# Performance work log

Hardware: AMD Instinct MI355X
Metric: run time of the kernel (lower is better)

Reference implementation:

```python
import jax, jax.numpy as jnp
import numpy as np

H, SK, SV, PK, PV = 12, 16, 16, 4, 8
SCALAR_DIM, PAIR_DIM = 384, 128
SIZES = [SK*H, SK*H, SV*H, PK*H*3, PK*H*3, PV*H*3]  # qkv split sizes
N_LOGITS = 3
SS = (N_LOGITS * SK) ** -0.5                 # scalar logit scale
PS = (N_LOGITS * PK * 4.5) ** -0.5           # point logit scale
PBS = N_LOGITS ** -0.5                       # pair bias scale
EPS = 1e-8


def setup_inputs() -> dict:
    key = jax.random.key(0)
    ks = jax.random.split(key, 16)
    b, n = 1, 768
    scalar_feats = jax.random.normal(ks[0], (b, n, SCALAR_DIM), jnp.float32)
    pair_feats = jax.random.normal(ks[1], (b, n, n, PAIR_DIM), jnp.float32)
    rotations = jax.random.normal(ks[2], (b, n, 3, 3), jnp.float32)
    translations = jax.random.normal(ks[3], (b, n, 3), jnp.float32)
    mask = jnp.ones((b, n), dtype=bool)
    d_qkv = sum(SIZES)
    sc = SCALAR_DIM ** -0.5
    Wqkv = jax.random.normal(ks[4], (SCALAR_DIM, d_qkv), jnp.float32) * sc
    Wpb = jax.random.normal(ks[5], (PAIR_DIM, H), jnp.float32) * PAIR_DIM ** -0.5
    point_weights = jnp.full((1, H, 1, 1), float(np.log(np.e - 1.0)), jnp.float32)
    dim_out = H * (PAIR_DIM + SV + 4 * PV)  # 2112
    Wout = jax.random.normal(ks[6], (dim_out, SCALAR_DIM), jnp.float32) * dim_out ** -0.5
    bout = jnp.zeros((SCALAR_DIM,), jnp.float32)
    Wp1 = jax.random.normal(ks[7], (3 * H, PAIR_DIM), jnp.float32) * (3 * H) ** -0.5
    bp1 = jnp.zeros((PAIR_DIM,), jnp.float32)
    Wp2 = jax.random.normal(ks[8], (PAIR_DIM, PAIR_DIM), jnp.float32) * PAIR_DIM ** -0.5
    bp2 = jnp.zeros((PAIR_DIM,), jnp.float32)
    return dict(scalar_feats=scalar_feats, pair_feats=pair_feats, rotations=rotations,
                translations=translations, mask=mask, Wqkv=Wqkv, Wpb=Wpb,
                point_weights=point_weights, Wout=Wout, bout=bout,
                Wp1=Wp1, bp1=bp1, Wp2=Wp2, bp2=bp2)


def _heads(x, b, n, d):
    # b n (h d) -> b h n d
    return x.reshape(b, n, H, d).transpose(0, 2, 1, 3)


def _merge(x):
    # b h n d -> b n (h d)
    b, h, n, d = x.shape
    return x.transpose(0, 2, 1, 3).reshape(b, n, h * d)


def ipa_forward(scalar_feats, pair_feats, rotations, translations, mask,
                Wqkv, Wpb, point_weights, Wout, bout, Wp1, bp1, Wp2, bp2):
    b, n, _ = scalar_feats.shape
    qkv = scalar_feats @ Wqkv
    offs = np.cumsum([0] + SIZES)
    qs, ks_, vs, qp, kp, vp = [qkv[..., offs[i]:offs[i + 1]] for i in range(6)]
    qs, ks_, vs = _heads(qs, b, n, SK), _heads(ks_, b, n, SK), _heads(vs, b, n, SV)

    def to_global_points(p, d):
        p = p.reshape(b, n, H * d, 3)                       # ... (d c) -> ... d c
        p = jnp.einsum('bixy,bidy->bidx', rotations, p) + translations[:, :, None, :]
        return p.reshape(b, n, H, d, 3).transpose(0, 2, 1, 3, 4)  # b h n d 3

    qp, kp = to_global_points(qp, PK), to_global_points(kp, PK)
    vp = to_global_points(vp, PV)

    scalar_logits = jnp.einsum('bhid,bhjd->bhij', qs, ks_)
    pair_bias = jnp.einsum('bijd,dh->bhij', pair_feats, Wpb)
    point_logits = jnp.einsum('bhidc,bhjdc->bhij', qp, kp) * jax.nn.softplus(point_weights)

    m2 = mask[:, None, :, None] & mask[:, None, None, :]    # b 1 i j
    neg = -jnp.finfo(scalar_logits.dtype).max
    scalar_logits = jnp.where(m2, scalar_logits, neg)
    point_logits = jnp.where(m2, point_logits, neg)
    pair_bias = jnp.where(m2, pair_bias, neg)

    attn = jax.nn.softmax(SS * scalar_logits + PS * point_logits + PBS * pair_bias, axis=-1)

    res_scalar = jnp.einsum('bhij,bhjd->bhid', attn, vs)
    res_pair = jnp.einsum('bhij,bijd->bhid', attn, pair_feats)
    res_pts = jnp.einsum('bhij,bhjdc->bhidc', attn, vp)
    # inverse rigid: R^T (p - t)
    local = jnp.einsum('biyx,bhidy->bhidx', rotations,
                       res_pts - translations[:, None, :, None, :])
    pts_norm = jnp.sqrt(jnp.sum(local ** 2, axis=-1) + EPS)  # safe_norm

    feats = jnp.concatenate([
        _merge(res_scalar),                                   # b n h*SV
        _merge(res_pair),                                     # b n h*PAIR_DIM
        _merge(local.reshape(b, H, n, PV * 3)),               # b n h*PV*3
        _merge(pts_norm),                                     # b n h*PV
    ], axis=-1)
    scalar_out = feats @ Wout + bout

    edge = jnp.concatenate([attn,
                            jax.nn.softmax(point_logits, axis=-1),
                            jax.nn.softmax(scalar_logits, axis=-1)], axis=1)
    edge = edge.transpose(0, 2, 3, 1)                         # b i j (3h)
    pair_out = jax.nn.gelu(edge @ Wp1 + bp1, approximate=False) @ Wp2 + bp2
    return scalar_out, pair_out


def reference(scalar_feats, pair_feats, rotations, translations, mask,
              Wqkv, Wpb, point_weights, Wout, bout, Wp1, bp1, Wp2, bp2):
    return ipa_forward(scalar_feats, pair_feats, rotations, translations, mask,
                       Wqkv, Wpb, point_weights, Wout, bout, Wp1, bp1, Wp2, bp2)
```

## Files before the change

### kernel.cpp

```cpp
#include <hip/hip_runtime.h>
#include <hip/hip_bf16.h>
#include <math.h>

#define NRES 768
#define NH 12
#define DQKV 1152
#define PAIRD 128
#define SCD 384
#define DOUTF 2112

#define SS_C 0.14433756729740643f
#define PS_C 0.13608276348795434f
#define PBS_C 0.5773502691896258f

typedef __attribute__((ext_vector_type(4))) float f32x4;
typedef __attribute__((ext_vector_type(8))) short s16x8;

__device__ __forceinline__ unsigned short f2bf(float x) {
  union { float f; unsigned u; } v; v.f = x;
  unsigned r = (v.u + 0x7fffu + ((v.u >> 16) & 1u)) >> 16;
  return (unsigned short)r;
}
__device__ __forceinline__ float bf2f(unsigned short h) {
  union { unsigned u; float f; } v; v.u = (unsigned)h << 16;
  return v.f;
}

__global__ __launch_bounds__(256) void gemm_bf16(
    const unsigned short* __restrict__ A, const unsigned short* __restrict__ Bt,
    const float* __restrict__ bias, float* __restrict__ C,
    int M, int Nn, int K)
{
  __shared__ __align__(16) unsigned short A_lds[64][72];
  __shared__ __align__(16) unsigned short B_lds[64][72];
  int m0 = blockIdx.y * 64, n0 = blockIdx.x * 64;
  int t = threadIdx.x;
  int lane = t & 63, w = t >> 6;
  int n15 = lane & 15, q = lane >> 4;
  f32x4 acc[4];
#pragma unroll
  for (int nt = 0; nt < 4; ++nt) acc[nt] = (f32x4){0.f, 0.f, 0.f, 0.f};
  for (int k0 = 0; k0 < K; k0 += 64) {
    __syncthreads();
#pragma unroll
    for (int u = 0; u < 2; ++u) {
      int idx = t + u * 256;
      int r = idx >> 3, c = (idx & 7) * 8;
      *(s16x8*)&A_lds[r][c] = *(const s16x8*)&A[(size_t)(m0 + r) * K + k0 + c];
      *(s16x8*)&B_lds[r][c] = *(const s16x8*)&Bt[(size_t)(n0 + r) * K + k0 + c];
    }
    __syncthreads();
#pragma unroll
    for (int ks = 0; ks < 2; ++ks) {
      s16x8 af = *(const s16x8*)&A_lds[w * 16 + n15][ks * 32 + q * 8];
#pragma unroll
      for (int nt = 0; nt < 4; ++nt) {
        s16x8 bf = *(const s16x8*)&B_lds[nt * 16 + n15][ks * 32 + q * 8];
        acc[nt] = __builtin_amdgcn_mfma_f32_16x16x32_bf16(af, bf, acc[nt], 0, 0, 0);
      }
    }
  }
#pragma unroll
  for (int nt = 0; nt < 4; ++nt) {
    int n = n0 + nt * 16 + n15;
    float bv = bias ? bias[n] : 0.f;
#pragma unroll
    for (int r = 0; r < 4; ++r) {
      int m = m0 + w * 16 + q * 4 + r;
      C[(size_t)m * Nn + n] = acc[nt][r] + bv;
    }
  }
}

__global__ __launch_bounds__(256) void prep_wqkv_kernel(
    const float* __restrict__ W, unsigned short* __restrict__ Bt)
{
  __shared__ float tile[32][33];
  int k0 = blockIdx.x * 32, n0 = blockIdx.y * 32;
  int t = threadIdx.x;
  int x = t & 31, y = t >> 5;
#pragma unroll
  for (int r = 0; r < 32; r += 8)
    tile[y + r][x] = W[(size_t)(k0 + y + r) * DQKV + n0 + x];
  __syncthreads();
#pragma unroll
  for (int r = 0; r < 32; r += 8) {
    float v = tile[x][y + r];
    unsigned short hi = f2bf(v);
    unsigned short lo = f2bf(v - bf2f(hi));
    size_t nrow = (size_t)(n0 + y + r) * 1152;
    Bt[nrow + k0 + x]       = hi;
    Bt[nrow + 384 + k0 + x] = lo;
    Bt[nrow + 768 + k0 + x] = hi;
  }
}

__global__ __launch_bounds__(128) void prep_a_kernel(
    const float* __restrict__ A, unsigned short* __restrict__ Ap)
{
  int i = blockIdx.x, t = threadIdx.x;
#pragma unroll
  for (int p = 0; p < 3; ++p) {
    int c = t + p * 128;
    float v = A[(size_t)i * SCD + c];
    unsigned short hi = f2bf(v);
    unsigned short lo = f2bf(v - bf2f(hi));
    size_t row = (size_t)i * 1152;
    Ap[row + c]       = hi;
    Ap[row + 384 + c] = hi;
    Ap[row + 768 + c] = lo;
  }
}

__global__ __launch_bounds__(256) void wt_kernel(
    const float* __restrict__ W, unsigned short* __restrict__ Wt)
{
  __shared__ float tile[32][33];
  int k0 = blockIdx.x * 32, n0 = blockIdx.y * 32;
  int t = threadIdx.x;
  int x = t & 31, y = t >> 5;
#pragma unroll
  for (int r = 0; r < 32; r += 8)
    tile[y + r][x] = W[(size_t)(k0 + y + r) * SCD + n0 + x];
  __syncthreads();
#pragma unroll
  for (int r = 0; r < 32; r += 8)
    Wt[(size_t)(n0 + y + r) * DOUTF + k0 + x] = f2bf(tile[x][y + r]);
}

__global__ __launch_bounds__(192) void points_kernel(
    const float* __restrict__ qkv, const float* __restrict__ rot,
    const float* __restrict__ trans, float* __restrict__ QP,
    float* __restrict__ KP, float* __restrict__ VP, float* __restrict__ Kq)
{
  int i = blockIdx.x;
  int t = threadIdx.x;
  const float* R = rot + (size_t)i * 9;
  const float* T = trans + (size_t)i * 3;
  int base; float* outp;
  if (t < 48) { int h = t >> 2, d = t & 3; base = 576 + (h * 4 + d) * 3;
    outp = QP + ((size_t)h * NRES + i) * 12 + d * 3; }
  else if (t < 96) { int u = t - 48; int h = u >> 2, d = u & 3; base = 720 + (h * 4 + d) * 3;
    outp = KP + ((size_t)h * NRES + i) * 12 + d * 3; }
  else { int u = t - 96; int h = u >> 3, d = u & 7; base = 864 + (h * 8 + d) * 3;
    outp = VP + ((size_t)h * NRES + i) * 24 + d * 3; }
  const float* p = qkv + (size_t)i * DQKV + base;
  float p0 = p[0], p1 = p[1], p2 = p[2];
#pragma unroll
  for (int x = 0; x < 3; ++x)
    outp[x] = R[x * 3 + 0] * p0 + R[x * 3 + 1] * p1 + R[x * 3 + 2] * p2 + T[x];
  {
    int h = t >> 4, d = t & 15;
    Kq[((size_t)h * NRES + i) * 16 + d] = qkv[(size_t)i * DQKV + 192 + h * 16 + d];
  }
}

__global__ __launch_bounds__(256) void vt_kernel(
    const float* __restrict__ qkv, const float* __restrict__ VP,
    unsigned short* __restrict__ Vt)
{
  int b = blockIdx.x;
  int h = b / 48, o = b % 48;
  int t = threadIdx.x;
  for (int p = 0; p < 3; ++p) {
    int j = p * 256 + t;
    float v;
    if (o < 16) v = qkv[(size_t)j * DQKV + 384 + h * 16 + o];
    else if (o < 40) v = VP[((size_t)h * NRES + j) * 24 + (o - 16)];
    else v = 0.f;
    Vt[((size_t)h * 48 + o) * NRES + j] = f2bf(v);
  }
}

__global__ __launch_bounds__(256) void pair_bias_kernel(
    const float* __restrict__ pair, const float* __restrict__ Wpb,
    float* __restrict__ Lb, unsigned short* __restrict__ pair_b)
{
  __shared__ __align__(16) unsigned short Bt[64][136];
  int jt = blockIdx.x, i = blockIdx.y;
  int j0 = jt * 64;
  int t = threadIdx.x;
  int lane = t & 63, w = t >> 6;
  int n15 = lane & 15, q = lane >> 4;
  s16x8 wf[4];
#pragma unroll
  for (int ks = 0; ks < 4; ++ks) {
#pragma unroll
    for (int jj = 0; jj < 8; ++jj) {
      int k = ks * 32 + q * 8 + jj;
      float v = (n15 < 12) ? Wpb[k * 12 + n15] : 0.f;
      wf[ks][jj] = (short)f2bf(v);
    }
  }
  {
    int dq = t & 31, jb = t >> 5;
    for (int p = 0; p < 8; ++p) {
      int j = p * 8 + jb;
      float4 v = *(const float4*)(pair + ((size_t)i * NRES + j0 + j) * PAIRD + dq * 4);
      unsigned lo = (unsigned)f2bf(v.x) | ((unsigned)f2bf(v.y) << 16);
      unsigned hi = (unsigned)f2bf(v.z) | ((unsigned)f2bf(v.w) << 16);
      uint2 pk; pk.x = lo; pk.y = hi;
      *(uint2*)&Bt[j][dq * 4] = pk;
      *(uint2*)&pair_b[((size_t)i * NRES + j0 + j) * PAIRD + dq * 4] = pk;
    }
  }
  __syncthreads();
  f32x4 acc = {0.f, 0.f, 0.f, 0.f};
  int m = w * 16 + n15;
#pragma unroll
  for (int ks = 0; ks < 4; ++ks) {
    s16x8 af = *(const s16x8*)&Bt[m][ks * 32 + q * 8];
    acc = __builtin_amdgcn_mfma_f32_16x16x32_bf16(af, wf[ks], acc, 0, 0, 0);
  }
  if (n15 < 12) {
    int j = j0 + w * 16 + q * 4;
    float4 st; st.x = acc[0]; st.y = acc[1]; st.z = acc[2]; st.w = acc[3];
    *(float4*)(Lb + ((size_t)n15 * NRES + i) * NRES + j) = st;
  }
}

#define RL 4
__global__ __launch_bounds__(256) void logits_softmax_kernel(
    const float* __restrict__ qkv, const float* __restrict__ Kq,
    const float* __restrict__ QP, const float* __restrict__ KP,
    const float* __restrict__ pw, const float* __restrict__ Lb,
    unsigned short* __restrict__ attn_b, unsigned short* __restrict__ sp_b,
    unsigned short* __restrict__ ss_b)
{
  int it = blockIdx.x, h = blockIdx.y;
  int i0 = it * RL;
  int t = threadIdx.x;
  __shared__ float q_sh[RL][28];
  if (t < RL * 28) {
    int r = t / 28, c = t % 28;
    q_sh[r][c] = (c < 16) ? qkv[(size_t)(i0 + r) * DQKV + h * 16 + c]
                          : QP[((size_t)h * NRES + i0 + r) * 12 + (c - 16)];
  }
  __syncthreads();
  float spw = log1pf(expf(pw[h]));
  float s[RL][3], p[RL][3], c[RL][3];
#pragma unroll
  for (int e = 0; e < 3; ++e) {
    int j = t + e * 256;
    float kr[16];
    const float* kq = Kq + ((size_t)h * NRES + j) * 16;
    *(float4*)&kr[0]  = *(const float4*)(kq + 0);
    *(float4*)&kr[4]  = *(const float4*)(kq + 4);
    *(float4*)&kr[8]  = *(const float4*)(kq + 8);
    *(float4*)&kr[12] = *(const float4*)(kq + 12);
    float kp[12];
    const float* kpp = KP + ((size_t)h * NRES + j) * 12;
    *(float4*)&kp[0] = *(const float4*)(kpp + 0);
    *(float4*)&kp[4] = *(const float4*)(kpp + 4);
    *(float4*)&kp[8] = *(const float4*)(kpp + 8);
#pragma unroll
    for (int r = 0; r < RL; ++r) {
      float sv = 0.f;
#pragma unroll
      for (int d = 0; d < 16; ++d) sv += q_sh[r][d] * kr[d];
      float pv = 0.f;
#pragma unroll
      for (int d = 0; d < 12; ++d) pv += q_sh[r][16 + d] * kp[d];
      pv *= spw;
      float bv = Lb[((size_t)h * NRES + i0 + r) * NRES + j];
      s[r][e] = sv; p[r][e] = pv;
      c[r][e] = SS_C * sv + PS_C * pv + PBS_C * bv;
    }
  }
  __shared__ float redm[4][RL][3];
  __shared__ float redsu[4][RL][3];
  int wv = t >> 6;
#pragma unroll
  for (int r = 0; r < RL; ++r) {
    float ms = fmaxf(fmaxf(s[r][0], s[r][1]), s[r][2]);
    float mp = fmaxf(fmaxf(p[r][0], p[r][1]), p[r][2]);
    float mc = fmaxf(fmaxf(c[r][0], c[r][1]), c[r][2]);
#pragma unroll
    for (int o = 32; o > 0; o >>= 1) {
      ms = fmaxf(ms, __shfl_down(ms, o));
      mp = fmaxf(mp, __shfl_down(mp, o));
      mc = fmaxf(mc, __shfl_down(mc, o));
    }
    if ((t & 63) == 0) { redm[wv][r][0] = ms; redm[wv][r][1] = mp; redm[wv][r][2] = mc; }
  }
  __syncthreads();
  float Ms[RL], Mp[RL], Mc[RL];
#pragma unroll
  for (int r = 0; r < RL; ++r) {
    Ms[r] = fmaxf(fmaxf(redm[0][r][0], redm[1][r][0]), fmaxf(redm[2][r][0], redm[3][r][0]));
    Mp[r] = fmaxf(fmaxf(redm[0][r][1], redm[1][r][1]), fmaxf(redm[2][r][1], redm[3][r][1]));
    Mc[r] = fmaxf(fmaxf(redm[0][r][2], redm[1][r][2]), fmaxf(redm[2][r][2], redm[3][r][2]));
  }
#pragma unroll
  for (int r = 0; r < RL; ++r) {
    float sums = 0.f, sump = 0.f, sumc = 0.f;
#pragma unroll
    for (int e = 0; e < 3; ++e) {
      float es = expf(s[r][e] - Ms[r]); s[r][e] = es; sums += es;
      float ep = expf(p[r][e] - Mp[r]); p[r][e] = ep; sump += ep;
      float ec = expf(c[r][e] - Mc[r]); c[r][e] = ec; sumc += ec;
    }
#pragma unroll
    for (int o = 32; o > 0; o >>= 1) {
      sums += __shfl_down(sums, o);
      sump += __shfl_down(sump, o);
      sumc += __shfl_down(sumc, o);
    }
    if ((t & 63) == 0) { redsu[wv][r][0] = sums; redsu[wv][r][1] = sump; redsu[wv][r][2] = sumc; }
  }
  __syncthreads();
#pragma unroll
  for (int r = 0; r < RL; ++r) {
    float rs = 1.f / (redsu[0][r][0] + redsu[1][r][0] + redsu[2][r][0] + redsu[3][r][0]);
    float rp = 1.f / (redsu[0][r][1] + redsu[1][r][1] + redsu[2][r][1] + redsu[3][r][1]);
    float rc = 1.f / (redsu[0][r][2] + redsu[1][r][2] + redsu[2][r][2] + redsu[3][r][2]);
    size_t off = ((size_t)h * NRES + i0 + r) * NRES;
#pragma unroll
    for (int e = 0; e < 3; ++e) {
      int j = t + e * 256;
      ss_b[off + j]   = f2bf(s[r][e] * rs);
      sp_b[off + j]   = f2bf(p[r][e] * rp);
      attn_b[off + j] = f2bf(c[r][e] * rc);
    }
  }
}

__global__ __launch_bounds__(192) void res_sv_kernel(
    const unsigned short* __restrict__ attn, const unsigned short* __restrict__ Vt,
    float* __restrict__ res_sv)
{
  __shared__ __align__(16) unsigned short A_lds[16][72];
  __shared__ __align__(16) unsigned short B_lds[48][72];
  int it = blockIdx.x, h = blockIdx.y;
  int i0 = it * 16;
  int t = threadIdx.x;
  int lane = t & 63, w = t >> 6;
  int n15 = lane & 15, q = lane >> 4;
  f32x4 acc = {0.f, 0.f, 0.f, 0.f};
  for (int jt = 0; jt < 12; ++jt) {
    int j0 = jt * 64;
    __syncthreads();
    for (int idx = t; idx < 512; idx += 192) {
      int r = idx >> 5, j2 = idx & 31;
      *(unsigned*)&A_lds[r][j2 * 2] =
          *(const unsigned*)&attn[((size_t)h * NRES + i0 + r) * NRES + j0 + j2 * 2];
    }
    for (int idx = t; idx < 1536; idx += 192) {
      int o = idx >> 5, j2 = idx & 31;
      *(unsigned*)&B_lds[o][j2 * 2] =
          *(const unsigned*)&Vt[((size_t)h * 48 + o) * NRES + j0 + j2 * 2];
    }
    __syncthreads();
#pragma unroll
    for (int ks = 0; ks < 2; ++ks) {
      s16x8 af = *(const s16x8*)&A_lds[n15][ks * 32 + q * 8];
      s16x8 bf = *(const s16x8*)&B_lds[w * 16 + n15][ks * 32 + q * 8];
      acc = __builtin_amdgcn_mfma_f32_16x16x32_bf16(af, bf, acc, 0, 0, 0);
    }
  }
  int o = w * 16 + n15;
  if (o < 40) {
#pragma unroll
    for (int r = 0; r < 4; ++r) {
      int i = i0 + q * 4 + r;
      res_sv[((size_t)h * NRES + i) * 40 + o] = acc[r];
    }
  }
}

__global__ __launch_bounds__(256) void res_pair_kernel(
    const unsigned short* __restrict__ attn, const unsigned short* __restrict__ pair_b,
    float* __restrict__ res_pair)
{
  __shared__ __align__(16) unsigned short A_lds[16][72];
  __shared__ __align__(16) unsigned short B_lds[64][132];
  int i = blockIdx.x;
  int t = threadIdx.x;
  int lane = t & 63, w = t >> 6;
  int n15 = lane & 15, q = lane >> 4;
  for (int idx = t; idx < 4 * 72; idx += 256)
    A_lds[12 + idx / 72][idx % 72] = 0;
  f32x4 acc[2];
  acc[0] = (f32x4){0.f, 0.f, 0.f, 0.f};
  acc[1] = (f32x4){0.f, 0.f, 0.f, 0.f};
  for (int jt = 0; jt < 12; ++jt) {
    int j0 = jt * 64;
    __syncthreads();
    for (int idx = t; idx < 384; idx += 256) {
      int r = idx >> 5, j2 = idx & 31;
      *(unsigned*)&A_lds[r][j2 * 2] =
          *(const unsigned*)&attn[((size_t)r * NRES + i) * NRES + j0 + j2 * 2];
    }
    {
      int o8 = t & 15, jb = t >> 4;
#pragma unroll
      for (int p = 0; p < 4; ++p) {
        int j = p * 16 + jb;
        *(s16x8*)&B_lds[j][o8 * 8] =
            *(const s16x8*)&pair_b[((size_t)i * NRES + j0 + j) * PAIRD + o8 * 8];
      }
    }
    __syncthreads();
#pragma unroll
    for (int ks = 0; ks < 2; ++ks) {
      s16x8 af = *(const s16x8*)&A_lds[n15][ks * 32 + q * 8];
#pragma unroll
      for (int nt = 0; nt < 2; ++nt) {
        int o = (w * 2 + nt) * 16 + n15;
        s16x8 bf;
#pragma unroll
        for (int jj = 0; jj < 8; ++jj)
          bf[jj] = (short)B_lds[ks * 32 + q * 8 + jj][o];
        acc[nt] = __builtin_amdgcn_mfma_f32_16x16x32_bf16(af, bf, acc[nt], 0, 0, 0);
      }
    }
  }
#pragma unroll
  for (int nt = 0; nt < 2; ++nt) {
    int o = (w * 2 + nt) * 16 + n15;
#pragma unroll
    for (int r = 0; r < 4; ++r) {
      int hh = q * 4 + r;
      if (hh < 12)
        res_pair[((size_t)hh * NRES + i) * PAIRD + o] = acc[nt][r];
    }
  }
}

__global__ __launch_bounds__(256) void feats_kernel(
    const float* __restrict__ res_sv, const float* __restrict__ res_pair,
    const float* __restrict__ rot, const float* __restrict__ trans,
    unsigned short* __restrict__ feats)
{
  int i = blockIdx.x;
  int t = threadIdx.x;
  unsigned short* F = feats + (size_t)i * DOUTF;
  if (t < 192) {
    int h = t >> 4, d = t & 15;
    F[t] = f2bf(res_sv[((size_t)h * NRES + i) * 40 + d]);
  }
  for (int e = 0; e < 6; ++e) {
    int idx = e * 256 + t;
    int h = idx >> 7, o = idx & 127;
    F[192 + idx] = f2bf(res_pair[((size_t)h * NRES + i) * PAIRD + o]);
  }
  if (t < 96) {
    int h = t >> 3, d = t & 7;
    const float* R = rot + (size_t)i * 9;
    const float* T = trans + (size_t)i * 3;
    const float* pp = res_sv + ((size_t)h * NRES + i) * 40 + 16 + d * 3;
    float p0 = pp[0] - T[0], p1 = pp[1] - T[1], p2 = pp[2] - T[2];
    float l0 = R[0] * p0 + R[3] * p1 + R[6] * p2;
    float l1 = R[1] * p0 + R[4] * p1 + R[7] * p2;
    float l2 = R[2] * p0 + R[5] * p1 + R[8] * p2;
    F[1728 + h * 24 + d * 3 + 0] = f2bf(l0);
    F[1728 + h * 24 + d * 3 + 1] = f2bf(l1);
    F[1728 + h * 24 + d * 3 + 2] = f2bf(l2);
    F[2016 + h * 8 + d] = f2bf(sqrtf(l0 * l0 + l1 * l1 + l2 * l2 + 1e-8f));
  }
}

__global__ __launch_bounds__(256) void mlp_kernel(
    const unsigned short* __restrict__ attn, const unsigned short* __restrict__ sp,
    const unsigned short* __restrict__ ss, const float* __restrict__ Wp1,
    const float* __restrict__ bp1, const float* __restrict__ Wp2,
    const float* __restrict__ bp2, float* __restrict__ out)
{
  __shared__ __align__(16) unsigned short E_lds[64][72];
  __shared__ __align__(16) unsigned short A_lds[64][136];
  int t = threadIdx.x;
  int lane = t & 63, w = t >> 6;
  int n15 = lane & 15, q = lane >> 4;
  for (int idx = t; idx < 64 * 28; idx += 256) {
    int j = idx / 28, k = 36 + idx % 28;
    E_lds[j][k] = 0;
  }
  s16x8 w1f[2][2], w2f[4][2];
#pragma unroll
  for (int ks = 0; ks < 2; ++ks)
#pragma unroll
    for (int nt = 0; nt < 2; ++nt) {
      int nn = (w * 2 + nt) * 16 + n15;
#pragma unroll
      for (int jj = 0; jj < 8; ++jj) {
        int k = ks * 32 + q * 8 + jj;
        w1f[ks][nt][jj] = (k < 36) ? (short)f2bf(Wp1[(size_t)k * 128 + nn]) : (short)0;
      }
    }
#pragma unroll
  for (int ks = 0; ks < 4; ++ks)
#pragma unroll
    for (int nt = 0; nt < 2; ++nt) {
      int nn = (w * 2 + nt) * 16 + n15;
#pragma unroll
      for (int jj = 0; jj < 8; ++jj) {
        int k = ks * 32 + q * 8 + jj;
        w2f[ks][nt][jj] = (short)f2bf(Wp2[(size_t)k * 128 + nn]);
      }
    }
  float b1v[2], b2v[2];
#pragma unroll
  for (int nt = 0; nt < 2; ++nt) {
    int nn = (w * 2 + nt) * 16 + n15;
    b1v[nt] = bp1[nn];
    b2v[nt] = bp2[nn];
  }
  const unsigned short* bufs[3] = {attn, sp, ss};
  for (int tile = blockIdx.x; tile < NRES * 12; tile += gridDim.x) {
    int i = tile / 12, j0 = (tile % 12) * 64;
    __syncthreads();
    {
      int j = t & 63, cb = t >> 6;
#pragma unroll
      for (int p = 0; p < 9; ++p) {
        int cc = cb * 9 + p;
        int hh = cc % 12;
        const unsigned short* src = bufs[cc / 12];
        E_lds[j][cc] = src[((size_t)hh * NRES + i) * NRES + j0 + j];
      }
    }
    __syncthreads();
    f32x4 c1[4][2];
#pragma unroll
    for (int mt = 0; mt < 4; ++mt) {
#pragma unroll
      for (int nt = 0; nt < 2; ++nt) c1[mt][nt] = (f32x4){0.f, 0.f, 0.f, 0.f};
#pragma unroll
      for (int ks = 0; ks < 2; ++ks) {
        s16x8 af = *(const s16x8*)&E_lds[mt * 16 + n15][ks * 32 + q * 8];
#pragma unroll
        for (int nt = 0; nt < 2; ++nt)
          c1[mt][nt] = __builtin_amdgcn_mfma_f32_16x16x32_bf16(af, w1f[ks][nt], c1[mt][nt], 0, 0, 0);
      }
    }
#pragma unroll
    for (int mt = 0; mt < 4; ++mt)
#pragma unroll
      for (int nt = 0; nt < 2; ++nt) {
        int o = (w * 2 + nt) * 16 + n15;
#pragma unroll
        for (int r = 0; r < 4; ++r) {
          float x = c1[mt][nt][r] + b1v[nt];
          float g = 0.5f * x * (1.f + erff(x * 0.70710678118654752f));
          A_lds[mt * 16 + q * 4 + r][o] = f2bf(g);
        }
      }
    __syncthreads();
    f32x4 c2[4][2];
#pragma unroll
    for (int mt = 0; mt < 4; ++mt) {
#pragma unroll
      for (int nt = 0; nt < 2; ++nt) c2[mt][nt] = (f32x4){0.f, 0.f, 0.f, 0.f};
#pragma unroll
      for (int ks = 0; ks < 4; ++ks) {
        s16x8 af = *(const s16x8*)&A_lds[mt * 16 + n15][ks * 32 + q * 8];
#pragma unroll
        for (int nt = 0; nt < 2; ++nt)
          c2[mt][nt] = __builtin_amdgcn_mfma_f32_16x16x32_bf16(af, w2f[ks][nt], c2[mt][nt], 0, 0, 0);
      }
    }
#pragma unroll
    for (int mt = 0; mt < 4; ++mt)
#pragma unroll
      for (int nt = 0; nt < 2; ++nt) {
        int o = (w * 2 + nt) * 16 + n15;
        int jb = j0 + mt * 16 + q * 4;
#pragma unroll
        for (int r = 0; r < 4; ++r)
          out[((size_t)i * NRES + jb + r) * PAIRD + o] = c2[mt][nt][r] + b2v[nt];
      }
  }
}

extern "C" void kernel_launch(void* const* d_in, const int* in_sizes, int n_in,
                              void* d_out, int out_size, void* d_ws, size_t ws_size,
                              hipStream_t stream) {
  const float* scalar_feats = (const float*)d_in[0];
  const float* pair  = (const float*)d_in[1];
  const float* rot   = (const float*)d_in[2];
  const float* trans = (const float*)d_in[3];
  const float* Wqkv  = (const float*)d_in[5];
  const float* Wpb   = (const float*)d_in[6];
  const float* pw    = (const float*)d_in[7];
  const float* Wout  = (const float*)d_in[8];
  const float* bout  = (const float*)d_in[9];
  const float* Wp1   = (const float*)d_in[10];
  const float* bp1   = (const float*)d_in[11];
  const float* Wp2   = (const float*)d_in[12];
  const float* bp2   = (const float*)d_in[13];
  float* out = (float*)d_out;
  float* ws = (float*)d_ws;

  float* qkv = ws;
  float* QP  = ws + 884736;
  float* KP  = ws + 995328;
  float* VP  = ws + 1105920;
  unsigned short* Vt = (unsigned short*)(ws + 1327104);
  float* Lb  = ws + 1548288;
  unsigned short* attn_b = (unsigned short*)(ws + 8626176);
  unsigned short* sp_b   = (unsigned short*)(ws + 12165120);
  unsigned short* ss_b   = (unsigned short*)(ws + 15704064);
  float* res_sv   = ws + 19243008;
  float* res_pair = ws + 19611648;
  unsigned short* feats_b = (unsigned short*)(ws + 20791296);
  unsigned short* Wout_t  = (unsigned short*)(ws + 21602304);
  float* Kq = ws + 22007808;
  unsigned short* Aprime  = (unsigned short*)(ws + 22155264);
  unsigned short* Wqkv_t  = (unsigned short*)(ws + 22597632);
  unsigned short* pair_b  = (unsigned short*)(ws + 23261184);

  prep_wqkv_kernel<<<dim3(SCD / 32, DQKV / 32), 256, 0, stream>>>(Wqkv, Wqkv_t);
  prep_a_kernel<<<NRES, 128, 0, stream>>>(scalar_feats, Aprime);
  gemm_bf16<<<dim3(DQKV / 64, NRES / 64), 256, 0, stream>>>(
      Aprime, Wqkv_t, nullptr, qkv, NRES, DQKV, 1152);
  points_kernel<<<NRES, 192, 0, stream>>>(qkv, rot, trans, QP, KP, VP, Kq);
  vt_kernel<<<576, 256, 0, stream>>>(qkv, VP, Vt);
  pair_bias_kernel<<<dim3(12, NRES), 256, 0, stream>>>(pair, Wpb, Lb, pair_b);
  logits_softmax_kernel<<<dim3(NRES / RL, 12), 256, 0, stream>>>(
      qkv, Kq, QP, KP, pw, Lb, attn_b, sp_b, ss_b);
  res_sv_kernel<<<dim3(48, 12), 192, 0, stream>>>(attn_b, Vt, res_sv);
  res_pair_kernel<<<NRES, 256, 0, stream>>>(attn_b, pair_b, res_pair);
  feats_kernel<<<NRES, 256, 0, stream>>>(res_sv, res_pair, rot, trans, feats_b);
  wt_kernel<<<dim3(DOUTF / 32, SCD / 32), 256, 0, stream>>>(Wout, Wout_t);
  gemm_bf16<<<dim3(SCD / 64, NRES / 64), 256, 0, stream>>>(
      feats_b, Wout_t, bout, out, NRES, SCD, DOUTF);
  mlp_kernel<<<2048, 256, 0, stream>>>(attn_b, sp_b, ss_b, Wp1, bp1, Wp2, bp2, out + 294912);
}
```

Baseline: 916.8 us.

## Transpose pair_b layout, prefetch MLP edge tiles, use fast exp and erf

```diff
diff --git a/kernel.cpp b/kernel.cpp
--- a/kernel.cpp
+++ b/kernel.cpp
@@ -24,6 +24,18 @@
 __device__ __forceinline__ float bf2f(unsigned short h) {
   union { unsigned u; float f; } v; v.u = (unsigned)h << 16;
   return v.f;
+}
+
+__device__ __forceinline__ float gelu_f(float x) {
+  float z = x * 0.70710678118654752f;
+  float az = fabsf(z);
+  float t = __builtin_amdgcn_rcpf(1.f + 0.3275911f * az);
+  float poly = t * (0.254829592f + t * (-0.284496736f +
+               t * (1.421413741f + t * (-1.453152027f + t * 1.061405429f))));
+  float e = __expf(-az * az);
+  float erfv = 1.f - poly * e;
+  erfv = (z < 0.f) ? -erfv : erfv;
+  return 0.5f * x * (1.f + erfv);
 }
 
 __global__ __launch_bounds__(256) void gemm_bf16(
@@ -174,7 +186,7 @@
 
 __global__ __launch_bounds__(256) void pair_bias_kernel(
     const float* __restrict__ pair, const float* __restrict__ Wpb,
-    float* __restrict__ Lb, unsigned short* __restrict__ pair_b)
+    float* __restrict__ Lb, unsigned short* __restrict__ pair_bT)
 {
   __shared__ __align__(16) unsigned short Bt[64][136];
   int jt = blockIdx.x, i = blockIdx.y;
@@ -201,7 +213,6 @@
       unsigned hi = (unsigned)f2bf(v.z) | ((unsigned)f2bf(v.w) << 16);
       uint2 pk; pk.x = lo; pk.y = hi;
       *(uint2*)&Bt[j][dq * 4] = pk;
-      *(uint2*)&pair_b[((size_t)i * NRES + j0 + j) * PAIRD + dq * 4] = pk;
     }
   }
   __syncthreads();
@@ -216,6 +227,17 @@
     int j = j0 + w * 16 + q * 4;
     float4 st; st.x = acc[0]; st.y = acc[1]; st.z = acc[2]; st.w = acc[3];
     *(float4*)(Lb + ((size_t)n15 * NRES + i) * NRES + j) = st;
+  }
+  {
+    int d = t >> 1, jh = t & 1;
+#pragma unroll
+    for (int c = 0; c < 4; ++c) {
+      s16x8 pk;
+#pragma unroll
+      for (int e = 0; e < 8; ++e)
+        pk[e] = (short)Bt[jh * 32 + c * 8 + e][d];
+      *(s16x8*)&pair_bT[((size_t)i * PAIRD + d) * NRES + j0 + jh * 32 + c * 8] = pk;
+    }
   }
 }
 
@@ -296,9 +318,9 @@
     float sums = 0.f, sump = 0.f, sumc = 0.f;
 #pragma unroll
     for (int e = 0; e < 3; ++e) {
-      float es = expf(s[r][e] - Ms[r]); s[r][e] = es; sums += es;
-      float ep = expf(p[r][e] - Mp[r]); p[r][e] = ep; sump += ep;
-      float ec = expf(c[r][e] - Mc[r]); c[r][e] = ec; sumc += ec;
+      float es = __expf(s[r][e] - Ms[r]); s[r][e] = es; sums += es;
+      float ep = __expf(p[r][e] - Mp[r]); p[r][e] = ep; sump += ep;
+      float ec = __expf(c[r][e] - Mc[r]); c[r][e] = ec; sumc += ec;
     }
 #pragma unroll
     for (int o = 32; o > 0; o >>= 1) {
@@ -369,11 +391,11 @@
 }
 
 __global__ __launch_bounds__(256) void res_pair_kernel(
-    const unsigned short* __restrict__ attn, const unsigned short* __restrict__ pair_b,
+    const unsigned short* __restrict__ attn, const unsigned short* __restrict__ pair_bT,
     float* __restrict__ res_pair)
 {
   __shared__ __align__(16) unsigned short A_lds[16][72];
-  __shared__ __align__(16) unsigned short B_lds[64][132];
+  __shared__ __align__(16) unsigned short B_lds[128][72];
   int i = blockIdx.x;
   int t = threadIdx.x;
   int lane = t & 63, w = t >> 6;
@@ -391,14 +413,12 @@
       *(unsigned*)&A_lds[r][j2 * 2] =
           *(const unsigned*)&attn[((size_t)r * NRES + i) * NRES + j0 + j2 * 2];
     }
-    {
-      int o8 = t & 15, jb = t >> 4;
-#pragma unroll
-      for (int p = 0; p < 4; ++p) {
-        int j = p * 16 + jb;
-        *(s16x8*)&B_lds[j][o8 * 8] =
-            *(const s16x8*)&pair_b[((size_t)i * NRES + j0 + j) * PAIRD + o8 * 8];
-      }
+#pragma unroll
+    for (int p = 0; p < 4; ++p) {
+      int chunk = t + p * 256;
+      int d = chunk >> 3, jc = (chunk & 7) * 8;
+      *(s16x8*)&B_lds[d][jc] =
+          *(const s16x8*)&pair_bT[((size_t)i * PAIRD + d) * NRES + j0 + jc];
     }
     __syncthreads();
 #pragma unroll
@@ -407,10 +427,7 @@
 #pragma unroll
       for (int nt = 0; nt < 2; ++nt) {
         int o = (w * 2 + nt) * 16 + n15;
-        s16x8 bf;
-#pragma unroll
-        for (int jj = 0; jj < 8; ++jj)
-          bf[jj] = (short)B_lds[ks * 32 + q * 8 + jj][o];
+        s16x8 bf = *(const s16x8*)&B_lds[o][ks * 32 + q * 8];
         acc[nt] = __builtin_amdgcn_mfma_f32_16x16x32_bf16(af, bf, acc[nt], 0, 0, 0);
       }
     }
@@ -466,14 +483,15 @@
     const float* __restrict__ bp1, const float* __restrict__ Wp2,
     const float* __restrict__ bp2, float* __restrict__ out)
 {
-  __shared__ __align__(16) unsigned short E_lds[64][72];
+  __shared__ __align__(16) unsigned short E_lds[2][64][72];
   __shared__ __align__(16) unsigned short A_lds[64][136];
   int t = threadIdx.x;
   int lane = t & 63, w = t >> 6;
   int n15 = lane & 15, q = lane >> 4;
-  for (int idx = t; idx < 64 * 28; idx += 256) {
-    int j = idx / 28, k = 36 + idx % 28;
-    E_lds[j][k] = 0;
+  for (int idx = t; idx < 64 * 28 * 2; idx += 256) {
+    int b = idx / (64 * 28);
+    int r = (idx / 28) % 64, k = 36 + idx % 28;
+    E_lds[b][r][k] = 0;
   }
   s16x8 w1f[2][2], w2f[4][2];
 #pragma unroll
@@ -506,20 +524,30 @@
     b2v[nt] = bp2[nn];
   }
   const unsigned short* bufs[3] = {attn, sp, ss};
-  for (int tile = blockIdx.x; tile < NRES * 12; tile += gridDim.x) {
+  const int NT = NRES * 12;
+  int ej = t & 63, ecb = t >> 6;
+  int tile = blockIdx.x;
+  int cur = 0;
+  if (tile < NT) {
     int i = tile / 12, j0 = (tile % 12) * 64;
-    __syncthreads();
-    {
-      int j = t & 63, cb = t >> 6;
+#pragma unroll
+    for (int p = 0; p < 9; ++p) {
+      int cc = ecb * 9 + p;
+      E_lds[0][ej][cc] = bufs[cc / 12][((size_t)(cc % 12) * NRES + i) * NRES + j0 + ej];
+    }
+  }
+  for (; tile < NT; tile += gridDim.x) {
+    int nxt = tile + gridDim.x;
+    __syncthreads();
+    unsigned short ev[9];
+    if (nxt < NT) {
+      int i2 = nxt / 12, j02 = (nxt % 12) * 64;
 #pragma unroll
       for (int p = 0; p < 9; ++p) {
-        int cc = cb * 9 + p;
-        int hh = cc % 12;
-        const unsigned short* src = bufs[cc / 12];
-        E_lds[j][cc] = src[((size_t)hh * NRES + i) * NRES + j0 + j];
-      }
-    }
-    __syncthreads();
+        int cc = ecb * 9 + p;
+        ev[p] = bufs[cc / 12][((size_t)(cc % 12) * NRES + i2) * NRES + j02 + ej];
+      }
+    }
     f32x4 c1[4][2];
 #pragma unroll
     for (int mt = 0; mt < 4; ++mt) {
@@ -527,7 +555,7 @@
       for (int nt = 0; nt < 2; ++nt) c1[mt][nt] = (f32x4){0.f, 0.f, 0.f, 0.f};
 #pragma unroll
       for (int ks = 0; ks < 2; ++ks) {
-        s16x8 af = *(const s16x8*)&E_lds[mt * 16 + n15][ks * 32 + q * 8];
+        s16x8 af = *(const s16x8*)&E_lds[cur][mt * 16 + n15][ks * 32 + q * 8];
 #pragma unroll
         for (int nt = 0; nt < 2; ++nt)
           c1[mt][nt] = __builtin_amdgcn_mfma_f32_16x16x32_bf16(af, w1f[ks][nt], c1[mt][nt], 0, 0, 0);
@@ -541,11 +569,16 @@
 #pragma unroll
         for (int r = 0; r < 4; ++r) {
           float x = c1[mt][nt][r] + b1v[nt];
-          float g = 0.5f * x * (1.f + erff(x * 0.70710678118654752f));
-          A_lds[mt * 16 + q * 4 + r][o] = f2bf(g);
+          A_lds[mt * 16 + q * 4 + r][o] = f2bf(gelu_f(x));
         }
       }
-    __syncthreads();
+    if (nxt < NT) {
+#pragma unroll
+      for (int p = 0; p < 9; ++p)
+        E_lds[cur ^ 1][ej][ecb * 9 + p] = ev[p];
+    }
+    __syncthreads();
+    int i = tile / 12, j0 = (tile % 12) * 64;
     f32x4 c2[4][2];
 #pragma unroll
     for (int mt = 0; mt < 4; ++mt) {
@@ -569,6 +602,7 @@
         for (int r = 0; r < 4; ++r)
           out[((size_t)i * NRES + jb + r) * PAIRD + o] = c2[mt][nt][r] + b2v[nt];
       }
+    cur ^= 1;
   }
 }
 
@@ -607,7 +641,7 @@
   float* Kq = ws + 22007808;
   unsigned short* Aprime  = (unsigned short*)(ws + 22155264);
   unsigned short* Wqkv_t  = (unsigned short*)(ws + 22597632);
-  unsigned short* pair_b  = (unsigned short*)(ws + 23261184);
+  unsigned short* pair_bT = (unsigned short*)(ws + 23261184);
 
   prep_wqkv_kernel<<<dim3(SCD / 32, DQKV / 32), 256, 0, stream>>>(Wqkv, Wqkv_t);
   prep_a_kernel<<<NRES, 128, 0, stream>>>(scalar_feats, Aprime);
@@ -615,14 +649,14 @@
       Aprime, Wqkv_t, nullptr, qkv, NRES, DQKV, 1152);
   points_kernel<<<NRES, 192, 0, stream>>>(qkv, rot, trans, QP, KP, VP, Kq);
   vt_kernel<<<576, 256, 0, stream>>>(qkv, VP, Vt);
-  pair_bias_kernel<<<dim3(12, NRES), 256, 0, stream>>>(pair, Wpb, Lb, pair_b);
+  pair_bias_kernel<<<dim3(12, NRES), 256, 0, stream>>>(pair, Wpb, Lb, pair_bT);
   logits_softmax_kernel<<<dim3(NRES / RL, 12), 256, 0, stream>>>(
       qkv, Kq, QP, KP, pw, Lb, attn_b, sp_b, ss_b);
   res_sv_kernel<<<dim3(48, 12), 192, 0, stream>>>(attn_b, Vt, res_sv);
-  res_pair_kernel<<<NRES, 256, 0, stream>>>(attn_b, pair_b, res_pair);
+  res_pair_kernel<<<NRES, 256, 0, stream>>>(attn_b, pair_bT, res_pair);
   feats_kernel<<<NRES, 256, 0, stream>>>(res_sv, res_pair, rot, trans, feats_b);
   wt_kernel<<<dim3(DOUTF / 32, SCD / 32), 256, 0, stream>>>(Wout, Wout_t);
   gemm_bf16<<<dim3(SCD / 64, NRES / 64), 256, 0, stream>>>(
       feats_b, Wout_t, bout, out, NRES, SCD, DOUTF);
-  mlp_kernel<<<2048, 256, 0, stream>>>(attn_b, sp_b, ss_b, Wp1, bp1, Wp2, bp2, out + 294912);
-}
+  mlp_kernel<<<2304, 256, 0, stream>>>(attn_b, sp_b, ss_b, Wp1, bp1, Wp2, bp2, out + 294912);
+}
```

Result: faster. 872.1 us (-4.9%).
